# Optimization experiments

Hardware: AMD Instinct MI355X
Metric: run time of the kernel (lower is better)

## Reference

```python
import jax, jax.numpy as jnp
import numpy as np
import math

B, S, D, H = 2, 2048, 2048, 16
DH = D // H  # 128


def _rope(x, cos, sin):
    # x: [b, s, h, dh]; cos/sin: [s, dh//2]
    b, s, h, dh = x.shape
    x2 = x.reshape(b, s, h, dh // 2, 2)
    a, bb = x2[..., 0], x2[..., 1]
    c = cos[None, :, None, :]
    sn = sin[None, :, None, :]
    out = jnp.stack([a * c - bb * sn, a * sn + bb * c], axis=-1)
    return out.reshape(b, s, h, dh)


def setup_inputs() -> dict:
    key = jax.random.key(0)
    ks = jax.random.split(key, 6)
    x = jax.random.normal(ks[0], (B, S, D), dtype=jnp.float32)
    # RoPE frequencies (theta=10000) as cos/sin of shape [S, DH//2]
    inv_freq = 1.0 / (10000.0 ** (np.arange(0, DH, 2, dtype=np.float32) / DH))
    t = np.arange(S, dtype=np.float32)
    ang = jnp.asarray(np.outer(t, inv_freq))  # [S, DH//2]
    freqs_cos = jnp.cos(ang)
    freqs_sin = jnp.sin(ang)
    # causal additive mask [1,1,S,S]
    neg = jnp.finfo(jnp.float32).min
    mask = jnp.where(jnp.tril(jnp.ones((S, S), dtype=bool)), 0.0, neg)[None, None]
    sc = 0.02
    wq = jax.random.normal(ks[1], (D, D), dtype=jnp.float32) * sc
    wk = jax.random.normal(ks[2], (D, D), dtype=jnp.float32) * sc
    wv = jax.random.normal(ks[3], (D, D), dtype=jnp.float32) * sc
    wo = jax.random.normal(ks[4], (D, D), dtype=jnp.float32) * sc
    return {"x": x, "freqs_cos": freqs_cos, "freqs_sin": freqs_sin,
            "mask": mask, "wq": wq, "wk": wk, "wv": wv, "wo": wo}


def reference(x, freqs_cos, freqs_sin, mask, wq, wk, wv, wo):
    b, s, _ = x.shape
    # torch Linear: y = x @ W.T (weights stored [out, in])
    xq = (x @ wq.T).reshape(b, s, H, DH)
    xk = (x @ wk.T).reshape(b, s, H, DH)
    xv = (x @ wv.T).reshape(b, s, H, DH)
    xq = _rope(xq, freqs_cos, freqs_sin)
    xk = _rope(xk, freqs_cos, freqs_sin)
    # [b, h, s, dh]
    q = xq.transpose(0, 2, 1, 3)
    k = xk.transpose(0, 2, 1, 3)
    v = xv.transpose(0, 2, 1, 3)
    scores = jnp.einsum('bhqd,bhkd->bhqk', q, k) / math.sqrt(DH)
    scores = scores + mask
    attn = jax.nn.softmax(scores, axis=-1)  # dropout p=0 (eval)
    out = jnp.einsum('bhqk,bhkd->bhqd', attn, v)
    out = out.transpose(0, 2, 1, 3).reshape(b, s, D)
    return out @ wo.T
```

## Files before the change

kernel.cpp:

```cpp
#include <hip/hip_runtime.h>

#define B_ 2
#define S_ 2048
#define D_ 2048
#define H_ 16
#define DH_ 128

typedef __bf16 bf16_8 __attribute__((ext_vector_type(8)));
typedef __bf16 bf16_4 __attribute__((ext_vector_type(4)));
typedef float f32x4 __attribute__((ext_vector_type(4)));

__device__ __forceinline__ f32x4 mfma16(bf16_8 a, bf16_8 b, f32x4 c) {
  return __builtin_amdgcn_mfma_f32_16x16x32_bf16(a, b, c, 0, 0, 0);
}

__device__ __forceinline__ bf16_8 load8(const float* p) {
  f32x4 a = *(const f32x4*)p;
  f32x4 b = *(const f32x4*)(p + 4);
  bf16_8 r;
  r[0] = (__bf16)a[0]; r[1] = (__bf16)a[1]; r[2] = (__bf16)a[2]; r[3] = (__bf16)a[3];
  r[4] = (__bf16)b[0]; r[5] = (__bf16)b[1]; r[6] = (__bf16)b[2]; r[7] = (__bf16)b[3];
  return r;
}

__device__ __forceinline__ void async16(const __bf16* g, __bf16* l) {
  __builtin_amdgcn_global_load_lds(
      (const __attribute__((address_space(1))) void*)g,
      (__attribute__((address_space(3))) void*)l, 16, 0, 0);
}

__global__ __launch_bounds__(256) void cvt_all(
    const float* __restrict__ x, const float* __restrict__ wq,
    const float* __restrict__ wk, const float* __restrict__ wv,
    const float* __restrict__ wo, __bf16* __restrict__ xb,
    __bf16* __restrict__ wqb, __bf16* __restrict__ wkb,
    __bf16* __restrict__ wvb, __bf16* __restrict__ wob)
{
  const int W8 = (D_ * D_) / 8;
  int i = blockIdx.x * 256 + threadIdx.x;
  if (i < 2 * W8) {
    *(bf16_8*)(xb + (size_t)i * 8) = load8(x + (size_t)i * 8);
  } else {
    int j = i - 2 * W8;
    int sel = j >> 19, off = j & (W8 - 1);
    const float* s = sel == 0 ? wq : sel == 1 ? wk : sel == 2 ? wv : wo;
    __bf16* d = sel == 0 ? wqb : sel == 1 ? wkb : sel == 2 ? wvb : wob;
    *(bf16_8*)(d + (size_t)off * 8) = load8(s + (size_t)off * 8);
  }
}

template <bool WB>
__global__ __launch_bounds__(256) void qkv_gemm(
    const __bf16* __restrict__ A,
    const float* __restrict__ wqf, const float* __restrict__ wkf,
    const float* __restrict__ wvf,
    const __bf16* __restrict__ wqb, const __bf16* __restrict__ wkb,
    const __bf16* __restrict__ wvb,
    const float* __restrict__ fc, const float* __restrict__ fs,
    __bf16* __restrict__ Qo, __bf16* __restrict__ Ko, __bf16* __restrict__ Vo)
{
  constexpr int WSW = WB ? 32 : 40;
  constexpr int STAGE_ELEMS = 128 * 32 + 128 * WSW;
  constexpr int TS_ELEMS = 64 * 136;
  constexpr int SM_ELEMS = STAGE_ELEMS > TS_ELEMS ? STAGE_ELEMS : TS_ELEMS;
  __shared__ __align__(16) __bf16 smem[SM_ELEMS];
  auto As = (__bf16(*)[32])smem;
  auto Ws = (__bf16(*)[WSW])(smem + 128 * 32);
  auto Ts = (__bf16(*)[136])smem;

  const int tid = threadIdx.x;
  const int wave = tid >> 6, lane = tid & 63;
  const int quad = lane >> 4, l16 = lane & 15;
  const int m0 = blockIdx.y * 128, n0 = blockIdx.x * 128;
  const int wsel = n0 >> 11, nloc = n0 & 2047;
  const int wm = (wave >> 1) * 64, wn = (wave & 1) * 64;
  const __bf16* agl = A + (size_t)(m0 + wave * 32 + (lane >> 2)) * 2048 + (lane & 3) * 8;
  f32x4 acc[4][4] = {};
  if (WB) {
    const __bf16* Wb = wsel == 0 ? wqb : wsel == 1 ? wkb : wvb;
    const __bf16* wgl = Wb + (size_t)(nloc + wave * 32 + (lane >> 2)) * 2048 + (lane & 3) * 8;
    for (int k0 = 0; k0 < 2048; k0 += 32) {
      __syncthreads();
      async16(agl + k0,             &As[wave * 32][0]);
      async16(agl + 16 * 2048 + k0, &As[wave * 32 + 16][0]);
      async16(wgl + k0,             &Ws[wave * 32][0]);
      async16(wgl + 16 * 2048 + k0, &Ws[wave * 32 + 16][0]);
      __syncthreads();
      bf16_8 af[4], bfr[4];
      for (int i = 0; i < 4; ++i) {
        af[i]  = *(const bf16_8*)&As[wm + i * 16 + l16][quad * 8];
        bfr[i] = *(const bf16_8*)&Ws[wn + i * 16 + l16][quad * 8];
      }
      for (int mi = 0; mi < 4; ++mi)
        for (int ni = 0; ni < 4; ++ni)
          acc[mi][ni] = mfma16(af[mi], bfr[ni], acc[mi][ni]);
    }
  } else {
    const float* W = wsel == 0 ? wqf : wsel == 1 ? wkf : wvf;
    const int srow = tid >> 1, scol = (tid & 1) * 16;
    const float* wg = W + (size_t)(nloc + srow) * 2048 + scol;
    for (int k0 = 0; k0 < 2048; k0 += 32) {
      __syncthreads();
      async16(agl + k0,             &As[wave * 32][0]);
      async16(agl + 16 * 2048 + k0, &As[wave * 32 + 16][0]);
      *(bf16_8*)&Ws[srow][scol]     = load8(wg + k0);
      *(bf16_8*)&Ws[srow][scol + 8] = load8(wg + k0 + 8);
      __syncthreads();
      bf16_8 af[4], bfr[4];
      for (int i = 0; i < 4; ++i) {
        af[i]  = *(const bf16_8*)&As[wm + i * 16 + l16][quad * 8];
        bfr[i] = *(const bf16_8*)&Ws[wn + i * 16 + l16][quad * 8];
      }
      for (int mi = 0; mi < 4; ++mi)
        for (int ni = 0; ni < 4; ++ni)
          acc[mi][ni] = mfma16(af[mi], bfr[ni], acc[mi][ni]);
    }
  }
  if (wsel < 2) {
    const float qscale = wsel == 0 ? 0.08838834764831845f * 1.4426950408889634f
                                   : 1.0f;
    __bf16* O = wsel == 0 ? Qo : Ko;
    for (int mi = 0; mi < 4; ++mi)
      for (int ni = 0; ni < 4; ++ni)
        for (int r = 0; r < 4; ++r) {
          int row = m0 + wm + mi * 16 + quad * 4 + r;
          int col = nloc + wn + ni * 16 + l16;
          float self = acc[mi][ni][r];
          float oth = __shfl_xor(self, 1);
          int s = row & (S_ - 1);
          int dh = col & (DH_ - 1);
          float c = fc[s * (DH_ / 2) + (dh >> 1)];
          float sn = fs[s * (DH_ / 2) + (dh >> 1)];
          float o = (dh & 1) ? (oth * sn + self * c) : (self * c - oth * sn);
          O[(size_t)row * 2048 + col] = (__bf16)(o * qscale);
        }
  } else {
    const int b = m0 >> 11, h = nloc >> 7;
    __bf16* vb = Vo + ((size_t)(b * H_ + h) * DH_) * S_ + (m0 & (S_ - 1));
    for (int p = 0; p < 2; ++p) {
      __syncthreads();
      if ((wn >> 6) == p) {
        for (int mi = 0; mi < 4; ++mi)
          for (int ni = 0; ni < 4; ++ni) {
            int cl = ni * 16 + l16;
            int rl = wm + mi * 16 + quad * 4;
            bf16_4 pk;
            for (int r = 0; r < 4; ++r) pk[r] = (__bf16)acc[mi][ni][r];
            *(bf16_4*)&Ts[cl][rl] = pk;
          }
      }
      __syncthreads();
      for (int i = 0; i < 4; ++i) {
        int dh = p * 64 + i * 16 + (tid >> 4);
        int sc = (tid & 15) * 8;
        *(bf16_8*)(vb + (size_t)dh * S_ + sc) = *(const bf16_8*)&Ts[dh - p * 64][sc];
      }
    }
  }
}

template <bool WB>
__global__ __launch_bounds__(256) void out_gemm(
    const __bf16* __restrict__ A, const float* __restrict__ Wf,
    const __bf16* __restrict__ Wb, float* __restrict__ C)
{
  __shared__ __bf16 As[128][32];
  __shared__ __bf16 Ws[128][WB ? 32 : 40];
  const int tid = threadIdx.x;
  const int wave = tid >> 6, lane = tid & 63;
  const int quad = lane >> 4, l16 = lane & 15;
  const int m0 = blockIdx.y * 128, n0 = blockIdx.x * 128;
  const int wm = (wave >> 1) * 64, wn = (wave & 1) * 64;
  const __bf16* agl = A + (size_t)(m0 + wave * 32 + (lane >> 2)) * 2048 + (lane & 3) * 8;
  f32x4 acc[4][4] = {};
  if (WB) {
    const __bf16* wgl = Wb + (size_t)(n0 + wave * 32 + (lane >> 2)) * 2048 + (lane & 3) * 8;
    for (int k0 = 0; k0 < 2048; k0 += 32) {
      __syncthreads();
      async16(agl + k0,             &As[wave * 32][0]);
      async16(agl + 16 * 2048 + k0, &As[wave * 32 + 16][0]);
      async16(wgl + k0,             &Ws[wave * 32][0]);
      async16(wgl + 16 * 2048 + k0, &Ws[wave * 32 + 16][0]);
      __syncthreads();
      bf16_8 af[4], bfr[4];
      for (int i = 0; i < 4; ++i) {
        af[i]  = *(const bf16_8*)&As[wm + i * 16 + l16][quad * 8];
        bfr[i] = *(const bf16_8*)&Ws[wn + i * 16 + l16][quad * 8];
      }
      for (int mi = 0; mi < 4; ++mi)
        for (int ni = 0; ni < 4; ++ni)
          acc[mi][ni] = mfma16(af[mi], bfr[ni], acc[mi][ni]);
    }
  } else {
    const int srow = tid >> 1, scol = (tid & 1) * 16;
    const float* wg = Wf + (size_t)(n0 + srow) * 2048 + scol;
    for (int k0 = 0; k0 < 2048; k0 += 32) {
      __syncthreads();
      async16(agl + k0,             &As[wave * 32][0]);
      async16(agl + 16 * 2048 + k0, &As[wave * 32 + 16][0]);
      *(bf16_8*)&Ws[srow][scol]     = load8(wg + k0);
      *(bf16_8*)&Ws[srow][scol + 8] = load8(wg + k0 + 8);
      __syncthreads();
      bf16_8 af[4], bfr[4];
      for (int i = 0; i < 4; ++i) {
        af[i]  = *(const bf16_8*)&As[wm + i * 16 + l16][quad * 8];
        bfr[i] = *(const bf16_8*)&Ws[wn + i * 16 + l16][quad * 8];
      }
      for (int mi = 0; mi < 4; ++mi)
        for (int ni = 0; ni < 4; ++ni)
          acc[mi][ni] = mfma16(af[mi], bfr[ni], acc[mi][ni]);
    }
  }
  for (int mi = 0; mi < 4; ++mi)
    for (int ni = 0; ni < 4; ++ni)
      for (int r = 0; r < 4; ++r) {
        int row = m0 + wm + mi * 16 + quad * 4 + r;
        int col = n0 + wn + ni * 16 + l16;
        C[(size_t)row * 2048 + col] = acc[mi][ni][r];
      }
}

__global__ __launch_bounds__(256) void attn_kernel(
    const __bf16* __restrict__ Q, const __bf16* __restrict__ K,
    const __bf16* __restrict__ Vt_g, __bf16* __restrict__ O)
{
  __shared__ __bf16 Ks[2][64 * 128];
  __shared__ __bf16 Vt[128 * 64];
  __shared__ __bf16 Ps[4][32][72];
  const int tid = threadIdx.x;
  const int wave = tid >> 6, lane = tid & 63;
  const int quad = lane >> 4, l16 = lane & 15;
  const int qt = gridDim.x - 1 - blockIdx.x;
  const int bh = blockIdx.y;
  const size_t base = (size_t)(bh >> 4) * S_ * D_ + (size_t)(bh & 15) * DH_;
  const size_t vtb = (size_t)bh * DH_ * S_;
  const int q0 = qt * 128;
  const int wmin = q0 + wave * 32;

  bf16_8 qf[2][4];
  for (int qs = 0; qs < 2; ++qs) {
    int qrow = wmin + qs * 16 + l16;
    for (int kk = 0; kk < 4; ++kk)
      qf[qs][kk] = *(const bf16_8*)(Q + base + (size_t)qrow * D_ + kk * 32 + quad * 8);
  }
  asm volatile("s_waitcnt vmcnt(0)" ::: "memory");

  const int krs = wave * 4 + (lane >> 4);
  const __bf16* kgl = K + base + (size_t)krs * D_ + ((lane & 15) ^ krs) * 8;
  const int vrs = wave * 8 + (lane >> 3);
  const __bf16* vgl = Vt_g + vtb + (size_t)vrs * S_ + ((lane & 7) ^ (lane >> 3)) * 8;

  f32x4 oacc[2][8] = {};
  float lsum[2][4] = {};
  const int nt = 2 * qt + 2;

  for (int p = 0; p < 4; ++p)
    async16(kgl + (size_t)(p * 16) * D_, Ks[0] + (p * 16 + wave * 4) * 128);
  for (int p = 0; p < 4; ++p)
    async16(vgl + (size_t)(p * 32) * S_, Vt + (p * 32 + wave * 8) * 64);

  int cur = 0;
  for (int kt = 0; kt < nt; ++kt) {
    const bool more = (kt + 1 < nt);
    if (more) {
      for (int p = 0; p < 4; ++p)
        async16(kgl + (size_t)((kt + 1) * 64 + p * 16) * D_,
                Ks[cur ^ 1] + (p * 16 + wave * 4) * 128);
      asm volatile("s_waitcnt vmcnt(8)" ::: "memory");
    } else {
      asm volatile("s_waitcnt vmcnt(4)" ::: "memory");
    }
    __builtin_amdgcn_s_barrier();
    asm volatile("" ::: "memory");

    const bool active = (kt * 64 <= wmin + 31);
    if (active) {
      const bool diag = (kt * 64 + 63 > wmin);
      const __bf16* ksb = Ks[cur];
      for (int n = 0; n < 4; ++n) {
        f32x4 s0 = {}, s1 = {};
        __builtin_amdgcn_s_setprio(1);
#pragma unroll
        for (int kk = 0; kk < 4; ++kk) {
          bf16_8 kf = *(const bf16_8*)&ksb[(n * 16 + l16) * 128 + (((kk * 4 + quad) ^ l16) * 8)];
          s0 = mfma16(qf[0][kk], kf, s0);
          s1 = mfma16(qf[1][kk], kf, s1);
        }
        __builtin_amdgcn_s_setprio(0);
#pragma unroll
        for (int qs = 0; qs < 2; ++qs) {
          f32x4 sv = qs ? s1 : s0;
          for (int r = 0; r < 4; ++r) {
            float v = sv[r];
            if (diag) {
              int qr = wmin + qs * 16 + quad * 4 + r;
              if (kt * 64 + n * 16 + l16 > qr) v = -INFINITY;
            }
            float p = exp2f(v);
            lsum[qs][r] += p;
            Ps[wave][qs * 16 + quad * 4 + r][n * 16 + l16] = (__bf16)p;
          }
        }
      }
    }

    if (more) asm volatile("s_waitcnt vmcnt(4)" ::: "memory");
    else      asm volatile("s_waitcnt vmcnt(0)" ::: "memory");
    __builtin_amdgcn_s_barrier();
    asm volatile("" ::: "memory");

    if (active) {
      bf16_8 pf0[2], pf1[2];
      for (int qs = 0; qs < 2; ++qs) {
        pf0[qs] = *(const bf16_8*)&Ps[wave][qs * 16 + l16][quad * 8];
        pf1[qs] = *(const bf16_8*)&Ps[wave][qs * 16 + l16][32 + quad * 8];
      }
      __builtin_amdgcn_s_setprio(1);
#pragma unroll
      for (int nc = 0; nc < 8; ++nc) {
        bf16_8 vf0 = *(const bf16_8*)&Vt[(nc * 16 + l16) * 64 + ((quad ^ (l16 & 7)) * 8)];
        bf16_8 vf1 = *(const bf16_8*)&Vt[(nc * 16 + l16) * 64 + (((quad + 4) ^ (l16 & 7)) * 8)];
        oacc[0][nc] = mfma16(pf0[0], vf0, oacc[0][nc]);
        oacc[0][nc] = mfma16(pf1[0], vf1, oacc[0][nc]);
        oacc[1][nc] = mfma16(pf0[1], vf0, oacc[1][nc]);
        oacc[1][nc] = mfma16(pf1[1], vf1, oacc[1][nc]);
      }
      __builtin_amdgcn_s_setprio(0);
    }

    asm volatile("s_waitcnt lgkmcnt(0)" ::: "memory");
    __builtin_amdgcn_s_barrier();
    asm volatile("" ::: "memory");
    if (more)
      for (int p = 0; p < 4; ++p)
        async16(vgl + (size_t)(p * 32) * S_ + (size_t)(kt + 1) * 64,
                Vt + (p * 32 + wave * 8) * 64);
    cur ^= 1;
  }

  for (int qs = 0; qs < 2; ++qs)
    for (int r = 0; r < 4; ++r) {
      float l = lsum[qs][r];
      l += __shfl_xor(l, 1);
      l += __shfl_xor(l, 2);
      l += __shfl_xor(l, 4);
      l += __shfl_xor(l, 8);
      float rinv = 1.f / l;
      int qr = wmin + qs * 16 + quad * 4 + r;
      for (int nc = 0; nc < 8; ++nc)
        O[base + (size_t)qr * D_ + nc * 16 + l16] = (__bf16)(oacc[qs][nc][r] * rinv);
    }
}

extern "C" void kernel_launch(void* const* d_in, const int* in_sizes, int n_in,
                              void* d_out, int out_size, void* d_ws, size_t ws_size,
                              hipStream_t stream)
{
  const float* x    = (const float*)d_in[0];
  const float* fcos = (const float*)d_in[1];
  const float* fsin = (const float*)d_in[2];
  const float* wq   = (const float*)d_in[4];
  const float* wk   = (const float*)d_in[5];
  const float* wv   = (const float*)d_in[6];
  const float* wo   = (const float*)d_in[7];
  float* out = (float*)d_out;

  const size_t T = (size_t)B_ * S_ * D_;
  const size_t W = (size_t)D_ * D_;
  __bf16* xb  = (__bf16*)d_ws;
  __bf16* qw  = xb + T;
  __bf16* kw  = qw + T;
  __bf16* vt  = kw + T;
  __bf16* wqb = vt + T;
  __bf16* wkb = wqb + W;
  __bf16* wvb = wkb + W;
  __bf16* wob = wvb + W;
  __bf16* ow  = xb;

  const bool wb = ws_size >= (4 * T + 4 * W) * sizeof(__bf16);
  const int W8 = (int)(W / 8);
  cvt_all<<<(wb ? 6 : 2) * W8 / 256, 256, 0, stream>>>(
      x, wq, wk, wv, wo, xb, wqb, wkb, wvb, wob);
  if (wb)
    qkv_gemm<true><<<dim3(48, 32), 256, 0, stream>>>(
        xb, nullptr, nullptr, nullptr, wqb, wkb, wvb, fcos, fsin, qw, kw, vt);
  else
    qkv_gemm<false><<<dim3(48, 32), 256, 0, stream>>>(
        xb, wq, wk, wv, nullptr, nullptr, nullptr, fcos, fsin, qw, kw, vt);
  attn_kernel<<<dim3(S_ / 128, B_ * H_), 256, 0, stream>>>(qw, kw, vt, ow);
  if (wb)
    out_gemm<true><<<dim3(16, 32), 256, 0, stream>>>(ow, nullptr, wob, out);
  else
    out_gemm<false><<<dim3(16, 32), 256, 0, stream>>>(ow, wo, nullptr, out);
}
```

Baseline: 453.8 us.

## Double-buffer async global-to-LDS loads in QKV and output GEMMs

Replaces the single-buffered K-loop in the bf16-weight paths of qkv_gemm and out_gemm with a two-stage ping-pong LDS pipeline. The next tile's async loads are issued before computing on the current one, and explicit vmcnt/lgkmcnt waits plus raw s_barrier replace the two __syncthreads per iteration. This aims to hide global-load latency behind the MFMA work. It doubles LDS use for staging, which may lower occupancy, and it depends on the hand-written waitcnt counts being correct.

After: 439.7 us. 3.1% less time.

```diff
diff --git a/kernel.cpp b/kernel.cpp
--- a/kernel.cpp
+++ b/kernel.cpp
@@ -59,14 +59,11 @@
     const float* __restrict__ fc, const float* __restrict__ fs,
     __bf16* __restrict__ Qo, __bf16* __restrict__ Ko, __bf16* __restrict__ Vo)
 {
-  constexpr int WSW = WB ? 32 : 40;
-  constexpr int STAGE_ELEMS = 128 * 32 + 128 * WSW;
+  constexpr int TILE = 128 * 32;
+  constexpr int STAGE_ELEMS = WB ? 4 * TILE : (128 * 32 + 128 * 40);
   constexpr int TS_ELEMS = 64 * 136;
   constexpr int SM_ELEMS = STAGE_ELEMS > TS_ELEMS ? STAGE_ELEMS : TS_ELEMS;
   __shared__ __align__(16) __bf16 smem[SM_ELEMS];
-  auto As = (__bf16(*)[32])smem;
-  auto Ws = (__bf16(*)[WSW])(smem + 128 * 32);
-  auto Ts = (__bf16(*)[136])smem;
 
   const int tid = threadIdx.x;
   const int wave = tid >> 6, lane = tid & 63;
@@ -79,23 +76,43 @@
   if (WB) {
     const __bf16* Wb = wsel == 0 ? wqb : wsel == 1 ? wkb : wvb;
     const __bf16* wgl = Wb + (size_t)(nloc + wave * 32 + (lane >> 2)) * 2048 + (lane & 3) * 8;
-    for (int k0 = 0; k0 < 2048; k0 += 32) {
-      __syncthreads();
-      async16(agl + k0,             &As[wave * 32][0]);
-      async16(agl + 16 * 2048 + k0, &As[wave * 32 + 16][0]);
-      async16(wgl + k0,             &Ws[wave * 32][0]);
-      async16(wgl + 16 * 2048 + k0, &Ws[wave * 32 + 16][0]);
-      __syncthreads();
+    auto STAGE = [&](int k0, int p) {
+      __bf16* ab = smem + p * TILE + (wave * 32) * 32;
+      __bf16* wb2 = smem + 2 * TILE + p * TILE + (wave * 32) * 32;
+      async16(agl + k0,             ab);
+      async16(agl + 16 * 2048 + k0, ab + 16 * 32);
+      async16(wgl + k0,             wb2);
+      async16(wgl + 16 * 2048 + k0, wb2 + 16 * 32);
+    };
+    STAGE(0, 0);
+#pragma unroll 2
+    for (int it = 0; it < 64; ++it) {
+      const int p = it & 1;
+      if (it + 1 < 64) {
+        STAGE((it + 1) * 32, p ^ 1);
+        asm volatile("s_waitcnt vmcnt(4)" ::: "memory");
+      } else {
+        asm volatile("s_waitcnt vmcnt(0)" ::: "memory");
+      }
+      __builtin_amdgcn_s_barrier();
+      asm volatile("" ::: "memory");
+      const __bf16* Ab = smem + p * TILE;
+      const __bf16* Wbuf = smem + 2 * TILE + p * TILE;
       bf16_8 af[4], bfr[4];
       for (int i = 0; i < 4; ++i) {
-        af[i]  = *(const bf16_8*)&As[wm + i * 16 + l16][quad * 8];
-        bfr[i] = *(const bf16_8*)&Ws[wn + i * 16 + l16][quad * 8];
+        af[i]  = *(const bf16_8*)(Ab   + (wm + i * 16 + l16) * 32 + quad * 8);
+        bfr[i] = *(const bf16_8*)(Wbuf + (wn + i * 16 + l16) * 32 + quad * 8);
       }
       for (int mi = 0; mi < 4; ++mi)
         for (int ni = 0; ni < 4; ++ni)
           acc[mi][ni] = mfma16(af[mi], bfr[ni], acc[mi][ni]);
+      asm volatile("s_waitcnt lgkmcnt(0)" ::: "memory");
+      __builtin_amdgcn_s_barrier();
+      asm volatile("" ::: "memory");
     }
   } else {
+    auto As = (__bf16(*)[32])smem;
+    auto Ws = (__bf16(*)[40])(smem + 128 * 32);
     const float* W = wsel == 0 ? wqf : wsel == 1 ? wkf : wvf;
     const int srow = tid >> 1, scol = (tid & 1) * 16;
     const float* wg = W + (size_t)(nloc + srow) * 2048 + scol;
@@ -135,6 +152,7 @@
           O[(size_t)row * 2048 + col] = (__bf16)(o * qscale);
         }
   } else {
+    auto Ts = (__bf16(*)[136])smem;
     const int b = m0 >> 11, h = nloc >> 7;
     __bf16* vb = Vo + ((size_t)(b * H_ + h) * DH_) * S_ + (m0 & (S_ - 1));
     for (int p = 0; p < 2; ++p) {
@@ -164,8 +182,9 @@
     const __bf16* __restrict__ A, const float* __restrict__ Wf,
     const __bf16* __restrict__ Wb, float* __restrict__ C)
 {
-  __shared__ __bf16 As[128][32];
-  __shared__ __bf16 Ws[128][WB ? 32 : 40];
+  constexpr int TILE = 128 * 32;
+  constexpr int SM_ELEMS = WB ? 4 * TILE : (128 * 32 + 128 * 40);
+  __shared__ __align__(16) __bf16 smem[SM_ELEMS];
   const int tid = threadIdx.x;
   const int wave = tid >> 6, lane = tid & 63;
   const int quad = lane >> 4, l16 = lane & 15;
@@ -175,23 +194,43 @@
   f32x4 acc[4][4] = {};
   if (WB) {
     const __bf16* wgl = Wb + (size_t)(n0 + wave * 32 + (lane >> 2)) * 2048 + (lane & 3) * 8;
-    for (int k0 = 0; k0 < 2048; k0 += 32) {
-      __syncthreads();
-      async16(agl + k0,             &As[wave * 32][0]);
-      async16(agl + 16 * 2048 + k0, &As[wave * 32 + 16][0]);
-      async16(wgl + k0,             &Ws[wave * 32][0]);
-      async16(wgl + 16 * 2048 + k0, &Ws[wave * 32 + 16][0]);
-      __syncthreads();
+    auto STAGE = [&](int k0, int p) {
+      __bf16* ab = smem + p * TILE + (wave * 32) * 32;
+      __bf16* wb2 = smem + 2 * TILE + p * TILE + (wave * 32) * 32;
+      async16(agl + k0,             ab);
+      async16(agl + 16 * 2048 + k0, ab + 16 * 32);
+      async16(wgl + k0,             wb2);
+      async16(wgl + 16 * 2048 + k0, wb2 + 16 * 32);
+    };
+    STAGE(0, 0);
+#pragma unroll 2
+    for (int it = 0; it < 64; ++it) {
+      const int p = it & 1;
+      if (it + 1 < 64) {
+        STAGE((it + 1) * 32, p ^ 1);
+        asm volatile("s_waitcnt vmcnt(4)" ::: "memory");
+      } else {
+        asm volatile("s_waitcnt vmcnt(0)" ::: "memory");
+      }
+      __builtin_amdgcn_s_barrier();
+      asm volatile("" ::: "memory");
+      const __bf16* Ab = smem + p * TILE;
+      const __bf16* Wbuf = smem + 2 * TILE + p * TILE;
       bf16_8 af[4], bfr[4];
       for (int i = 0; i < 4; ++i) {
-        af[i]  = *(const bf16_8*)&As[wm + i * 16 + l16][quad * 8];
-        bfr[i] = *(const bf16_8*)&Ws[wn + i * 16 + l16][quad * 8];
+        af[i]  = *(const bf16_8*)(Ab   + (wm + i * 16 + l16) * 32 + quad * 8);
+        bfr[i] = *(const bf16_8*)(Wbuf + (wn + i * 16 + l16) * 32 + quad * 8);
       }
       for (int mi = 0; mi < 4; ++mi)
         for (int ni = 0; ni < 4; ++ni)
           acc[mi][ni] = mfma16(af[mi], bfr[ni], acc[mi][ni]);
+      asm volatile("s_waitcnt lgkmcnt(0)" ::: "memory");
+      __builtin_amdgcn_s_barrier();
+      asm volatile("" ::: "memory");
     }
   } else {
+    auto As = (__bf16(*)[32])smem;
+    auto Ws = (__bf16(*)[40])(smem + 128 * 32);
     const int srow = tid >> 1, scol = (tid & 1) * 16;
     const float* wg = Wf + (size_t)(n0 + srow) * 2048 + scol;
     for (int k0 = 0; k0 < 2048; k0 += 32) {
```
